# Performance work log

Hardware: AMD Instinct MI355X
Metric: run time of the kernel (lower is better)

Reference implementation:

```python
import math
import jax, jax.numpy as jnp
import numpy as np

N_HEAD = 8
BLOCK_SIZE = 1024
LN_EPS = 1e-5


def _layer_norm(x, g, b):
    mu = jnp.mean(x, axis=-1, keepdims=True)
    var = jnp.var(x, axis=-1, keepdims=True)
    return (x - mu) * jax.lax.rsqrt(var + LN_EPS) * g + b


def _skew(QEr):
    # QEr: (B, nh, L, L) -> pad one zero column on the left, reshape, drop first row
    B, nh, nr, nc = QEr.shape
    padded = jnp.pad(QEr, ((0, 0), (0, 0), (0, 0), (1, 0)))  # (B, nh, nr, nc+1)
    reshaped = padded.reshape(B, nh, nc + 1, nr)
    return reshaped[:, :, 1:, :]  # (B, nh, nr, nc)


def _attn(x, W_qkv, b_qkv, W_o, b_o, Er):
    B, L, D = x.shape
    hs = D // N_HEAD
    qkv = x @ W_qkv + b_qkv  # (B, L, 3D)
    q, k, v = jnp.split(qkv, 3, axis=-1)
    # (B, nh, L, hs)
    q = q.reshape(B, L, N_HEAD, hs).transpose(0, 2, 1, 3)
    k = k.reshape(B, L, N_HEAD, hs).transpose(0, 2, 1, 3)
    v = v.reshape(B, L, N_HEAD, hs).transpose(0, 2, 1, 3)
    start = BLOCK_SIZE - L
    Er_t = Er[start:, :].T  # (hs, L)
    QEr = q @ Er_t  # (B, nh, L, L)
    Srel = _skew(QEr)
    scores = (jnp.einsum('bhqd,bhkd->bhqk', q, k) + Srel) * (1.0 / math.sqrt(hs))
    causal = jnp.tril(jnp.ones((L, L), dtype=bool))
    scores = jnp.where(causal, scores, jnp.float32(-jnp.inf))
    att = jax.nn.softmax(scores, axis=-1)
    y = jnp.einsum('bhqk,bhkd->bhqd', att, v)
    y = y.transpose(0, 2, 1, 3).reshape(B, L, D)
    return y @ W_o + b_o


def reference(x, W_qkv, b_qkv, W_o, b_o, Er, ln1_g, ln1_b, ln2_g, ln2_b,
              W_fc, b_fc, W_proj, b_proj):
    x = x + _attn(_layer_norm(x, ln1_g, ln1_b), W_qkv, b_qkv, W_o, b_o, Er)
    h = _layer_norm(x, ln2_g, ln2_b) @ W_fc + b_fc
    h = jax.nn.gelu(h, approximate=False)
    h = h @ W_proj + b_proj
    return x + h


def setup_inputs() -> dict:
    key = jax.random.key(0)
    ks = jax.random.split(key, 8)
    B, L, D, F = 8, 1024, 1024, 4096
    hs = D // N_HEAD
    s = lambda fan_in: 1.0 / math.sqrt(fan_in)
    return {
        'x': jax.random.normal(ks[0], (B, L, D), dtype=jnp.float32),
        'W_qkv': jax.random.normal(ks[1], (D, 3 * D), dtype=jnp.float32) * s(D),
        'b_qkv': jnp.zeros((3 * D,), dtype=jnp.float32),
        'W_o': jax.random.normal(ks[2], (D, D), dtype=jnp.float32) * s(D),
        'b_o': jnp.zeros((D,), dtype=jnp.float32),
        'Er': jax.random.normal(ks[3], (BLOCK_SIZE, hs), dtype=jnp.float32),
        'ln1_g': jnp.ones((D,), dtype=jnp.float32),
        'ln1_b': jnp.zeros((D,), dtype=jnp.float32),
        'ln2_g': jnp.ones((D,), dtype=jnp.float32),
        'ln2_b': jnp.zeros((D,), dtype=jnp.float32),
        'W_fc': jax.random.normal(ks[4], (D, F), dtype=jnp.float32) * s(D),
        'b_fc': jnp.zeros((F,), dtype=jnp.float32),
        'W_proj': jax.random.normal(ks[5], (F, D), dtype=jnp.float32) * s(F),
        'b_proj': jnp.zeros((D,), dtype=jnp.float32),
    }
```

## Files before the change

kernel.cpp:

```cpp
#include <hip/hip_runtime.h>
#include <hip/hip_bf16.h>
#include <math.h>

#define BB 8
#define LL 1024
#define DD 1024
#define FF 4096
#define NHH 8
#define HSS 128
#define SCALE 0.08838834764831845f
#define TRI(qi, kt) ((qi) * ((qi) + 1) / 2 + (kt))

typedef __bf16 bf16;
typedef __bf16 bf16x8 __attribute__((ext_vector_type(8)));
typedef float f32x4 __attribute__((ext_vector_type(4)));
typedef _Float16 f16;
typedef _Float16 f16x4 __attribute__((ext_vector_type(4)));

__device__ inline void async_copy16(const void* g, void* l) {
  __builtin_amdgcn_global_load_lds(
      (const __attribute__((address_space(1))) unsigned int*)g,
      (__attribute__((address_space(3))) unsigned int*)l, 16, 0, 0);
}

#define FENCE() asm volatile("" ::: "memory")
#define BARRIER() do { FENCE(); __builtin_amdgcn_s_barrier(); FENCE(); } while (0)
#define VMCNT0() asm volatile("s_waitcnt vmcnt(0)" ::: "memory")
#define VMCNT2() asm volatile("s_waitcnt vmcnt(2)" ::: "memory")
#define VMCNT4() asm volatile("s_waitcnt vmcnt(4)" ::: "memory")
#define VMCNT6() asm volatile("s_waitcnt vmcnt(6)" ::: "memory")

__global__ __launch_bounds__(256)
void prep_kernel(const float* __restrict__ Wq, const float* __restrict__ Wo,
                 const float* __restrict__ Wf, const float* __restrict__ Wp,
                 const float* __restrict__ Er, bf16* __restrict__ Wtq,
                 bf16* __restrict__ Wto, bf16* __restrict__ Wtf,
                 bf16* __restrict__ Wtp, bf16* __restrict__ ErP) {
  __shared__ float tile[32][33];
  int id = blockIdx.x, tid = threadIdx.x;
  if (id >= 12288) {
    int g = id - 12288;
    int l15 = tid & 15, quad = (tid >> 4) & 3, st = tid >> 6;
    const float* src = Er + (size_t)(g * 16 + l15) * HSS + st * 32 + quad * 8;
    bf16* dst = ErP + (size_t)g * 2048 + tid * 8;
#pragma unroll
    for (int j = 0; j < 8; j++) dst[j] = (bf16)src[j];
    return;
  }
  const float* W;
  bf16* Wt;
  int K, N, bx, by;
  if (id < 3072)      { W = Wq; Wt = Wtq; K = 1024; N = 3072; bx = id % 96;  by = id / 96; }
  else if (id < 4096) { id -= 3072; W = Wo; Wt = Wto; K = 1024; N = 1024; bx = id % 32;  by = id / 32; }
  else if (id < 8192) { id -= 4096; W = Wf; Wt = Wtf; K = 1024; N = 4096; bx = id % 128; by = id / 128; }
  else                { id -= 8192; W = Wp; Wt = Wtp; K = 4096; N = 1024; bx = id % 32;  by = id / 32; }
  int n0 = bx * 32, k0 = by * 32;
  int tx = tid & 31, ty = tid >> 5;
#pragma unroll
  for (int i = 0; i < 32; i += 8)
    tile[ty + i][tx] = W[(size_t)(k0 + ty + i) * N + n0 + tx];
  __syncthreads();
#pragma unroll
  for (int i = 0; i < 32; i += 8)
    Wt[(size_t)(n0 + ty + i) * K + k0 + tx] = (bf16)tile[tx][ty + i];
}

__global__ __launch_bounds__(256)
void ln_kernel(const float* __restrict__ x, const float* __restrict__ g,
               const float* __restrict__ bta, bf16* __restrict__ out) {
  int row = blockIdx.x;
  int tid = threadIdx.x;
  const float4 v = ((const float4*)(x + (size_t)row * DD))[tid];
  float s = v.x + v.y + v.z + v.w;
  float s2 = v.x * v.x + v.y * v.y + v.z * v.z + v.w * v.w;
#pragma unroll
  for (int o = 32; o > 0; o >>= 1) {
    s += __shfl_down(s, o);
    s2 += __shfl_down(s2, o);
  }
  __shared__ float a1[4], a2[4];
  int wave = tid >> 6;
  if ((tid & 63) == 0) { a1[wave] = s; a2[wave] = s2; }
  __syncthreads();
  s = a1[0] + a1[1] + a1[2] + a1[3];
  s2 = a2[0] + a2[1] + a2[2] + a2[3];
  float mu = s * (1.0f / DD);
  float rstd = rsqrtf(s2 * (1.0f / DD) - mu * mu + 1e-5f);
  float4 gv = ((const float4*)g)[tid];
  float4 bv = ((const float4*)bta)[tid];
  bf16* o4 = out + (size_t)row * DD + tid * 4;
  o4[0] = (bf16)((v.x - mu) * rstd * gv.x + bv.x);
  o4[1] = (bf16)((v.y - mu) * rstd * gv.y + bv.y);
  o4[2] = (bf16)((v.z - mu) * rstd * gv.z + bv.z);
  o4[3] = (bf16)((v.w - mu) * rstd * gv.w + bv.w);
}

template <int EPI>
__global__ __launch_bounds__(512)
void gemm256_kernel(const bf16* __restrict__ A, const bf16* __restrict__ Bt,
                    const float* __restrict__ bias, void* __restrict__ Cout,
                    int M, int N, int K) {
  __shared__ bf16 Als[2][256 * 64];
  __shared__ bf16 Bls[2][256 * 64];
  int tid = threadIdx.x;
  int wave = tid >> 6, lane = tid & 63;
  int l15 = lane & 15, quad = lane >> 4;
  int wmi = wave >> 2, wni = wave & 3;
  int m0 = blockIdx.y * 256, n0 = blockIdx.x * 256;

  int u0 = tid, u1 = tid + 512;
  int r0 = u0 >> 3, c0 = ((u0 & 7) ^ (r0 & 7)) << 3;
  int r1 = u1 >> 3, c1 = ((u1 & 7) ^ (r1 & 7)) << 3;
  const bf16* aB0 = A + (size_t)(m0 + r0) * K + c0;
  const bf16* aB1 = A + (size_t)(m0 + r1) * K + c1;
  const bf16* bB0 = Bt + (size_t)(n0 + r0) * K + c0;
  const bf16* bB1 = Bt + (size_t)(n0 + r1) * K + c1;
  int d0 = u0 * 8, d1 = u1 * 8;

  auto stageA = [&](int b, int h, int t) {
    size_t off = (size_t)h * 128 * K + (size_t)t * 64;
    async_copy16(aB0 + off, &Als[b][h * 8192 + d0]);
    async_copy16(aB1 + off, &Als[b][h * 8192 + d1]);
  };
  auto stageB = [&](int b, int h, int t) {
    size_t off = (size_t)h * 128 * K + (size_t)t * 64;
    async_copy16(bB0 + off, &Bls[b][h * 8192 + d0]);
    async_copy16(bB1 + off, &Bls[b][h * 8192 + d1]);
  };

  f32x4 acc[8][4] = {};
  bf16x8 af[2][4], bfr[2][2][2];

  auto readA = [&](int b, int qm) {
#pragma unroll
    for (int kk = 0; kk < 2; kk++)
#pragma unroll
      for (int mt = 0; mt < 4; mt++) {
        int ra = qm * 128 + wmi * 64 + mt * 16 + l15;
        af[kk][mt] = *(const bf16x8*)&Als[b][ra * 64 + (((kk * 4 + quad) ^ (ra & 7)) << 3)];
      }
  };
  auto readB = [&](int b, int qn) {
#pragma unroll
    for (int kk = 0; kk < 2; kk++)
#pragma unroll
      for (int nt = 0; nt < 2; nt++) {
        int rb = qn * 128 + wni * 32 + nt * 16 + l15;
        bfr[qn][kk][nt] = *(const bf16x8*)&Bls[b][rb * 64 + (((kk * 4 + quad) ^ (rb & 7)) << 3)];
      }
  };
  auto mfma16 = [&](int qm, int qn) {
    __builtin_amdgcn_s_setprio(1);
#pragma unroll
    for (int kk = 0; kk < 2; kk++)
#pragma unroll
      for (int mt = 0; mt < 4; mt++)
#pragma unroll
        for (int nt = 0; nt < 2; nt++)
          acc[qm * 4 + mt][qn * 2 + nt] = __builtin_amdgcn_mfma_f32_16x16x32_bf16(
              af[kk][mt], bfr[qn][kk][nt], acc[qm * 4 + mt][qn * 2 + nt], 0, 0, 0);
    __builtin_amdgcn_s_setprio(0);
  };

  int nk = K >> 6;
  stageA(0, 0, 0); stageB(0, 0, 0); stageB(0, 1, 0); stageA(0, 1, 0);
  stageA(1, 0, 1); stageB(1, 1, 1);
  VMCNT6();
  BARRIER();

  for (int t = 0; t < nk; t += 2) {
#pragma unroll
    for (int uu = 0; uu < 2; uu++) {
      const int tt = t + uu;
      const int cur = uu;
      readA(cur, 0); readB(cur, 0); readB(cur, 1);
      if (tt + 1 < nk) stageB(cur ^ 1, 0, tt + 1);
      BARRIER();
      mfma16(0, 0);
      BARRIER();
      if (tt + 1 < nk) stageA(cur ^ 1, 1, tt + 1);
      VMCNT6();
      BARRIER();
      mfma16(0, 1);
      BARRIER();
      readA(cur, 1);
      if (tt + 2 < nk) stageA(cur, 0, tt + 2);
      BARRIER();
      mfma16(1, 1);
      BARRIER();
      if (tt + 2 < nk) stageB(cur, 1, tt + 2);
      VMCNT6();
      BARRIER();
      mfma16(1, 0);
      BARRIER();
    }
  }

#pragma unroll
  for (int MT = 0; MT < 8; MT++) {
#pragma unroll
    for (int NT = 0; NT < 4; NT++) {
      int col = n0 + (NT >> 1) * 128 + wni * 32 + (NT & 1) * 16 + l15;
      float bv = bias[col];
#pragma unroll
      for (int r = 0; r < 4; r++) {
        int row = m0 + (MT >> 2) * 128 + wmi * 64 + (MT & 3) * 16 + quad * 4 + r;
        float v = acc[MT][NT][r] + bv;
        if (EPI == 1) v = 0.5f * v * (1.0f + erff(v * 0.7071067811865475f));
        ((bf16*)Cout)[(size_t)row * N + col] = (bf16)v;
      }
    }
  }
}

template <int EPI>
__global__ __launch_bounds__(512)
void gemm256n_kernel(const bf16* __restrict__ A, const bf16* __restrict__ Bt,
                     const float* __restrict__ bias, const float* __restrict__ res,
                     void* __restrict__ Cout, int M, int N, int K) {
  __shared__ bf16 Als[2][256 * 64];
  __shared__ bf16 Bls[2][128 * 64];
  int tid = threadIdx.x;
  int wave = tid >> 6, lane = tid & 63;
  int l15 = lane & 15, quad = lane >> 4;
  int wmi = wave >> 2, wni = wave & 3;
  int m0 = blockIdx.y * 256, n0 = blockIdx.x * 128;

  int u0 = tid, u1 = tid + 512;
  int r0 = u0 >> 3, c0 = ((u0 & 7) ^ (r0 & 7)) << 3;
  int r1 = u1 >> 3, c1 = ((u1 & 7) ^ (r1 & 7)) << 3;
  const bf16* aB0 = A + (size_t)(m0 + r0) * K + c0;
  const bf16* aB1 = A + (size_t)(m0 + r1) * K + c1;
  const bf16* bB0 = Bt + (size_t)(n0 + r0) * K + c0;
  const bf16* bB1 = Bt + (size_t)(n0 + r1) * K + c1;
  int d0 = u0 * 8, d1 = u1 * 8;

  auto stageA = [&](int b, int h, int t) {
    size_t off = (size_t)h * 128 * K + (size_t)t * 64;
    async_copy16(aB0 + off, &Als[b][h * 8192 + d0]);
    async_copy16(aB1 + off, &Als[b][h * 8192 + d1]);
  };
  auto stageB = [&](int b, int t) {
    size_t off = (size_t)t * 64;
    async_copy16(bB0 + off, &Bls[b][d0]);
    async_copy16(bB1 + off, &Bls[b][d1]);
  };

  f32x4 acc[8][2] = {};
  bf16x8 af[2][4], bfr[2][2];

  auto readA = [&](int b, int qm) {
#pragma unroll
    for (int kk = 0; kk < 2; kk++)
#pragma unroll
      for (int mt = 0; mt < 4; mt++) {
        int ra = qm * 128 + wmi * 64 + mt * 16 + l15;
        af[kk][mt] = *(const bf16x8*)&Als[b][ra * 64 + (((kk * 4 + quad) ^ (ra & 7)) << 3)];
      }
  };
  auto readB = [&](int b) {
#pragma unroll
    for (int kk = 0; kk < 2; kk++)
#pragma unroll
      for (int nt = 0; nt < 2; nt++) {
        int rb = wni * 32 + nt * 16 + l15;
        bfr[kk][nt] = *(const bf16x8*)&Bls[b][rb * 64 + (((kk * 4 + quad) ^ (rb & 7)) << 3)];
      }
  };
  auto mfma16 = [&](int qm) {
    __builtin_amdgcn_s_setprio(1);
#pragma unroll
    for (int kk = 0; kk < 2; kk++)
#pragma unroll
      for (int mt = 0; mt < 4; mt++)
#pragma unroll
        for (int nt = 0; nt < 2; nt++)
          acc[qm * 4 + mt][nt] = __builtin_amdgcn_mfma_f32_16x16x32_bf16(
              af[kk][mt], bfr[kk][nt], acc[qm * 4 + mt][nt], 0, 0, 0);
    __builtin_amdgcn_s_setprio(0);
  };

  int nk = K >> 6;
  stageB(0, 0); stageB(1, 1); stageA(0, 0, 0); stageA(0, 1, 0);
  VMCNT0();
  BARRIER();

  for (int t = 0; t < nk; t += 2) {
#pragma unroll
    for (int uu = 0; uu < 2; uu++) {
      const int tt = t + uu;
      const int cur = uu;
      readA(cur, 0); readB(cur);
      if (tt + 1 < nk) { stageA(cur ^ 1, 0, tt + 1); VMCNT4(); }
      else { VMCNT0(); }
      BARRIER();
      mfma16(0);
      BARRIER();
      readA(cur, 1);
      if (tt + 1 < nk) stageA(cur ^ 1, 1, tt + 1);
      if (tt + 2 < nk) { stageB(cur, tt + 2); VMCNT4(); }
      else { VMCNT2(); }
      BARRIER();
      mfma16(1);
      BARRIER();
    }
  }

#pragma unroll
  for (int MT = 0; MT < 8; MT++) {
#pragma unroll
    for (int NT = 0; NT < 2; NT++) {
      int col = n0 + wni * 32 + NT * 16 + l15;
      float bv = bias[col];
#pragma unroll
      for (int r = 0; r < 4; r++) {
        int row = m0 + (MT >> 2) * 128 + wmi * 64 + (MT & 3) * 16 + quad * 4 + r;
        float v = acc[MT][NT][r] + bv;
        if (EPI == 1) v = 0.5f * v * (1.0f + erff(v * 0.7071067811865475f));
        if (EPI == 2) {
          v += res[(size_t)row * N + col];
          ((float*)Cout)[(size_t)row * N + col] = v;
        } else {
          ((bf16*)Cout)[(size_t)row * N + col] = (bf16)v;
        }
      }
    }
  }
}

__global__ __launch_bounds__(256)
void pack_v_kernel(const bf16* __restrict__ qkv, bf16* __restrict__ Vpack) {
  __shared__ bf16 Vst[64][132];
  int kt = blockIdx.x, h = blockIdx.y, b = blockIdx.z;
  int tid = threadIdx.x;
  const size_t rs = 3 * DD;
  const bf16* vb = qkv + (size_t)b * LL * rs + (size_t)(kt * 64) * rs + 2 * DD + h * HSS;
  bf16* vp = Vpack + ((size_t)(b * NHH + h) * 16 + kt) * (128 * 64);
#pragma unroll
  for (int i = 0; i < 4; i++) {
    int u = i * 256 + tid;
    int kk = u >> 4, c = u & 15;
    *(bf16x8*)&Vst[kk][c * 8] = *(const bf16x8*)(vb + (size_t)kk * rs + c * 8);
  }
  __syncthreads();
#pragma unroll
  for (int i = 0; i < 4; i++) {
    int u = i * 256 + tid;
    int d = u >> 3, c = u & 7;
    bf16x8 t;
#pragma unroll
    for (int j = 0; j < 8; j++) t[j] = Vst[c * 8 + j][d];
    *(bf16x8*)(vp + d * 64 + ((c ^ (d & 7))) * 8) = t;
  }
}

__global__ __launch_bounds__(256)
void relband_kernel(const bf16* __restrict__ qkv, const bf16* __restrict__ ErP,
                    f16* __restrict__ band) {
  int tid = threadIdx.x, wave = tid >> 6, lane = tid & 63;
  int l15 = lane & 15, quad = lane >> 4;
  int h = blockIdx.y, b = blockIdx.z;
  const size_t rs = 3 * DD;
  const bf16* qbase = qkv + (size_t)b * LL * rs + h * HSS;
  f16* bbase = band + (size_t)(b * NHH + h) * (136 * 4096);

#pragma unroll 1
  for (int ph = 0; ph < 2; ph++) {
    int qb = ph ? 15 - blockIdx.x : blockIdx.x;
    int qw0 = qb * 64 + wave * 16;

    bf16x8 qf[4];
#pragma unroll
    for (int st = 0; st < 4; st++)
      qf[st] = *(const bf16x8*)(qbase + (size_t)(qw0 + l15) * rs + st * 32 + quad * 8);

#pragma unroll 1
    for (int kt = 0; kt <= qb; kt++) {
      int k0 = kt * 64;
      int kmax_off = qw0 + 15 - k0;
      int m_base = 1008 - qw0 + k0;
      int gb = m_base >> 4;
      int ntR = (kmax_off >> 4) + 1;
      if (ntR > 4) ntR = 4;

      f32x4 rr[5] = {};
      __builtin_amdgcn_s_setprio(1);
#pragma unroll
      for (int n = 0; n < 5; n++) {
        if (n <= ntR) {
          int g = gb + n;
          if (g > 63) g = 63;
          const bf16* ep = ErP + (size_t)g * 2048 + lane * 8;
#pragma unroll
          for (int st = 0; st < 4; st++) {
            bf16x8 ef = *(const bf16x8*)(ep + st * 512);
            rr[n] = __builtin_amdgcn_mfma_f32_16x16x32_bf16(qf[st], ef, rr[n], 0, 0, 0);
          }
        }
      }
      __builtin_amdgcn_s_setprio(0);

      f16x4 sf[4];
#pragma unroll
      for (int rg = 0; rg < 4; rg++) {
        int qloc = quad * 4 + rg;
        int tt = 15 - qloc + l15;
        int src = (lane & 48) | (tt & 15);
        float shv[5];
#pragma unroll
        for (int n = 0; n < 5; n++)
          shv[n] = (n <= ntR) ? __shfl(rr[n][rg], src) : 0.f;
#pragma unroll
        for (int nt = 0; nt < 4; nt++)
          sf[nt][rg] = (f16)((tt & 16) ? shv[nt + 1] : shv[nt]);
      }
      f16* tb = bbase + (size_t)TRI(qb, kt) * 4096;
#pragma unroll
      for (int nt = 0; nt < 4; nt++)
        if (nt * 16 <= kmax_off)
          *(f16x4*)(tb + (wave * 4 + nt) * 256 + l15 * 16 + quad * 4) = sf[nt];
    }
  }
}

__global__ __launch_bounds__(256)
void flash_kernel(const bf16* __restrict__ qkv, const bf16* __restrict__ Vpack,
                  const f16* __restrict__ band, bf16* __restrict__ y) {
  __shared__ bf16 Kls[2][64 * 128];
  __shared__ bf16 Vls[2][128 * 64];
  __shared__ bf16 Pls[4][16][72];

  int tid = threadIdx.x, wave = tid >> 6, lane = tid & 63;
  int l15 = lane & 15, quad = lane >> 4;
  int h = blockIdx.y, b = blockIdx.z;

  const size_t rs = 3 * DD;
  const bf16* qbase = qkv + (size_t)b * LL * rs + h * HSS;
  const bf16* kb = qbase + DD;
  const bf16* vp = Vpack + (size_t)(b * NHH + h) * 16 * (128 * 64);
  const f16* bnd = band + (size_t)(b * NHH + h) * (136 * 4096);

  size_t koff[4];
  int ldso[4];
#pragma unroll
  for (int i = 0; i < 4; i++) {
    int off = (wave * 4 + i) * 512 + lane * 8;
    int u = off >> 3;
    int kk = u >> 4, c = u & 15;
    koff[i] = (size_t)kk * rs + (size_t)(((c ^ kk) & 15) * 8);
    ldso[i] = off;
  }

  int buf = 0;
#pragma unroll 1
  for (int ph = 0; ph < 2; ph++) {
    int qb = ph ? 15 - blockIdx.x : blockIdx.x;
    int qw0 = qb * 64 + wave * 16;
    int nkt = qb + 1;

    bf16x8 qf[4];
#pragma unroll
    for (int st = 0; st < 4; st++)
      qf[st] = *(const bf16x8*)(qbase + (size_t)(qw0 + l15) * rs + st * 32 + quad * 8);

#pragma unroll
    for (int i = 0; i < 4; i++) {
      async_copy16(kb + koff[i], &Kls[buf][ldso[i]]);
      async_copy16(vp + ldso[i], &Vls[buf][ldso[i]]);
    }

    f32x4 o[8] = {};
    float mrow[4] = {-INFINITY, -INFINITY, -INFINITY, -INFINITY};
    float lrow[4] = {0.f, 0.f, 0.f, 0.f};

#pragma unroll 1
    for (int kt = 0; kt < nkt; kt++) {
      int k0 = kt * 64;
      int kmax_off = qw0 + 15 - k0;
      __syncthreads();

      const f16* tb = bnd + (size_t)TRI(qb, kt) * 4096;
      f16x4 srl[4] = {};
#pragma unroll
      for (int nt = 0; nt < 4; nt++)
        if (nt * 16 <= kmax_off)
          srl[nt] = *(const f16x4*)(tb + (wave * 4 + nt) * 256 + l15 * 16 + quad * 4);

      if (kt + 1 < nkt) {
        const bf16* ks = kb + (size_t)(kt + 1) * 64 * rs;
        const bf16* vs = vp + (size_t)(kt + 1) * (128 * 64);
#pragma unroll
        for (int i = 0; i < 4; i++) {
          async_copy16(ks + koff[i], &Kls[buf ^ 1][ldso[i]]);
          async_copy16(vs + ldso[i], &Vls[buf ^ 1][ldso[i]]);
        }
      }

      f32x4 sa[4] = {};
      __builtin_amdgcn_s_setprio(1);
#pragma unroll
      for (int nt = 0; nt < 4; nt++) {
        if (nt * 16 <= kmax_off) {
          int kk = nt * 16 + l15;
#pragma unroll
          for (int st = 0; st < 4; st++) {
            bf16x8 kf = *(const bf16x8*)&Kls[buf][kk * 128 + (((st * 4 + quad) ^ l15) & 15) * 8];
            sa[nt] = __builtin_amdgcn_mfma_f32_16x16x32_bf16(qf[st], kf, sa[nt], 0, 0, 0);
          }
        }
      }
      __builtin_amdgcn_s_setprio(0);

      float pmx[4] = {-INFINITY, -INFINITY, -INFINITY, -INFINITY};
#pragma unroll
      for (int nt = 0; nt < 4; nt++) {
        if (nt * 16 <= kmax_off) {
          int kg = k0 + nt * 16 + l15;
#pragma unroll
          for (int rg = 0; rg < 4; rg++) {
            int qg = qw0 + quad * 4 + rg;
            float v = (sa[nt][rg] + (float)srl[nt][rg]) * SCALE;
            v = (kg <= qg) ? v : -INFINITY;
            sa[nt][rg] = v;
            pmx[rg] = fmaxf(pmx[rg], v);
          }
        } else {
#pragma unroll
          for (int rg = 0; rg < 4; rg++) sa[nt][rg] = -INFINITY;
        }
      }

      float vmx[4];
      bool need = false;
#pragma unroll
      for (int rg = 0; rg < 4; rg++) {
        float v = pmx[rg];
        v = fmaxf(v, __shfl_xor(v, 1));
        v = fmaxf(v, __shfl_xor(v, 2));
        v = fmaxf(v, __shfl_xor(v, 4));
        v = fmaxf(v, __shfl_xor(v, 8));
        vmx[rg] = v;
        need = need || (v - mrow[rg] > 8.0f);
      }
      if (__any(need)) {
#pragma unroll
        for (int rg = 0; rg < 4; rg++) {
          float mnew = fmaxf(mrow[rg], vmx[rg]);
          float alpha = __expf(mrow[rg] - mnew);
          mrow[rg] = mnew;
          lrow[rg] *= alpha;
#pragma unroll
          for (int nt = 0; nt < 8; nt++) o[nt][rg] *= alpha;
        }
      }
#pragma unroll
      for (int rg = 0; rg < 4; rg++) pmx[rg] = mrow[rg];

      float ls[4] = {0.f, 0.f, 0.f, 0.f};
#pragma unroll
      for (int nt = 0; nt < 4; nt++)
#pragma unroll
        for (int rg = 0; rg < 4; rg++) {
          float p = __expf(sa[nt][rg] - pmx[rg]);
          ls[rg] += p;
          Pls[wave][quad * 4 + rg][nt * 16 + l15] = (bf16)p;
        }
#pragma unroll
      for (int rg = 0; rg < 4; rg++) {
        float v = ls[rg];
        v += __shfl_xor(v, 1);
        v += __shfl_xor(v, 2);
        v += __shfl_xor(v, 4);
        v += __shfl_xor(v, 8);
        lrow[rg] += v;
      }

      bf16x8 pf[2];
#pragma unroll
      for (int s2 = 0; s2 < 2; s2++)
        pf[s2] = *(const bf16x8*)&Pls[wave][l15][s2 * 32 + quad * 8];
      __builtin_amdgcn_s_setprio(1);
#pragma unroll
      for (int nt = 0; nt < 8; nt++) {
        int d = nt * 16 + l15;
#pragma unroll
        for (int s2 = 0; s2 < 2; s2++) {
          if (s2 * 32 <= kmax_off) {
            bf16x8 vf = *(const bf16x8*)&Vls[buf][d * 64 + (((s2 * 4 + quad) ^ (l15 & 7)) & 7) * 8];
            o[nt] = __builtin_amdgcn_mfma_f32_16x16x32_bf16(pf[s2], vf, o[nt], 0, 0, 0);
          }
        }
      }
      __builtin_amdgcn_s_setprio(0);
      buf ^= 1;
    }

#pragma unroll
    for (int rg = 0; rg < 4; rg++) {
      float inv = 1.0f / lrow[rg];
      int qg = qw0 + quad * 4 + rg;
      bf16* yr = y + ((size_t)b * LL + qg) * DD + h * HSS;
#pragma unroll
      for (int nt = 0; nt < 8; nt++) yr[nt * 16 + l15] = (bf16)(o[nt][rg] * inv);
    }
  }
}

extern "C" void kernel_launch(void* const* d_in, const int* in_sizes, int n_in,
                              void* d_out, int out_size, void* d_ws, size_t ws_size,
                              hipStream_t stream) {
  const float* x = (const float*)d_in[0];
  const float* W_qkv = (const float*)d_in[1];
  const float* b_qkv = (const float*)d_in[2];
  const float* W_o = (const float*)d_in[3];
  const float* b_o = (const float*)d_in[4];
  const float* Er = (const float*)d_in[5];
  const float* ln1_g = (const float*)d_in[6];
  const float* ln1_b = (const float*)d_in[7];
  const float* ln2_g = (const float*)d_in[8];
  const float* ln2_b = (const float*)d_in[9];
  const float* W_fc = (const float*)d_in[10];
  const float* b_fc = (const float*)d_in[11];
  const float* W_proj = (const float*)d_in[12];
  const float* b_proj = (const float*)d_in[13];
  float* out = (float*)d_out;

  char* p = (char*)d_ws;
  auto alloc = [&](size_t bytes) {
    char* r = p;
    p += (bytes + 255) & ~(size_t)255;
    return r;
  };
  bf16* Wt_qkv = (bf16*)alloc((size_t)3072 * 1024 * 2);
  bf16* Wt_o   = (bf16*)alloc((size_t)1024 * 1024 * 2);
  bf16* Wt_fc  = (bf16*)alloc((size_t)4096 * 1024 * 2);
  bf16* Wt_pr  = (bf16*)alloc((size_t)1024 * 4096 * 2);
  bf16* ErP    = (bf16*)alloc((size_t)1024 * 128 * 2);
  bf16* xn     = (bf16*)alloc((size_t)8192 * 1024 * 2);
  bf16* qkvb   = (bf16*)alloc((size_t)8192 * 3072 * 2);
  bf16* yb     = (bf16*)alloc((size_t)8192 * 1024 * 2);
  bf16* Vpack  = (bf16*)alloc((size_t)64 * 16 * 128 * 64 * 2);
  f16*  band   = (f16*)alloc((size_t)64 * 136 * 4096 * 2);
  float* x2    = (float*)band;
  bf16* hb     = qkvb;

  prep_kernel<<<12352, 256, 0, stream>>>(W_qkv, W_o, W_fc, W_proj, Er,
                                         Wt_qkv, Wt_o, Wt_fc, Wt_pr, ErP);

  ln_kernel<<<8192, 256, 0, stream>>>(x, ln1_g, ln1_b, xn);
  gemm256n_kernel<0><<<dim3(24, 32), 512, 0, stream>>>(xn, Wt_qkv, b_qkv, nullptr, qkvb, 8192, 3072, 1024);
  pack_v_kernel<<<dim3(16, 8, 8), 256, 0, stream>>>(qkvb, Vpack);
  relband_kernel<<<dim3(8, 8, 8), 256, 0, stream>>>(qkvb, ErP, band);
  flash_kernel<<<dim3(8, 8, 8), 256, 0, stream>>>(qkvb, Vpack, band, yb);
  gemm256n_kernel<2><<<dim3(8, 32), 512, 0, stream>>>(yb, Wt_o, b_o, x, x2, 8192, 1024, 1024);
  ln_kernel<<<8192, 256, 0, stream>>>(x2, ln2_g, ln2_b, xn);
  gemm256_kernel<1><<<dim3(16, 32), 512, 0, stream>>>(xn, Wt_fc, b_fc, hb, 8192, 4096, 1024);
  gemm256n_kernel<2><<<dim3(8, 32), 512, 0, stream>>>(hb, Wt_pr, b_proj, x2, out, 8192, 1024, 4096);
}
```

Before: 604.6 us.

## Fuse relative-position band computation into flash attention kernel

Removes the separate relband kernel, which computed the skewed Q·Er band and wrote it to global memory as f16. The flash kernel now loads Er tiles itself, runs extra MFMAs per key tile, and does the skew with lane shuffles in registers before masking and softmax. This drops the band write and read-back plus one launch, at the cost of more register pressure (20 extra bf16x8 fragments) and more work inside the attention loop, which may lower occupancy. x2 now gets its own buffer, since it no longer aliases the band.

```diff
diff --git a/kernel.cpp b/kernel.cpp
--- a/kernel.cpp
+++ b/kernel.cpp
@@ -355,36 +355,65 @@
 }
 
 __global__ __launch_bounds__(256)
-void relband_kernel(const bf16* __restrict__ qkv, const bf16* __restrict__ ErP,
-                    f16* __restrict__ band) {
+void flash_kernel(const bf16* __restrict__ qkv, const bf16* __restrict__ Vpack,
+                  const bf16* __restrict__ ErP, bf16* __restrict__ y) {
+  __shared__ bf16 Kls[2][64 * 128];
+  __shared__ bf16 Vls[2][128 * 64];
+  __shared__ bf16 Pls[4][16][72];
+
   int tid = threadIdx.x, wave = tid >> 6, lane = tid & 63;
   int l15 = lane & 15, quad = lane >> 4;
   int h = blockIdx.y, b = blockIdx.z;
+
   const size_t rs = 3 * DD;
   const bf16* qbase = qkv + (size_t)b * LL * rs + h * HSS;
-  f16* bbase = band + (size_t)(b * NHH + h) * (136 * 4096);
-
+  const bf16* kb = qbase + DD;
+  const bf16* vp = Vpack + (size_t)(b * NHH + h) * 16 * (128 * 64);
+
+  size_t koff[4];
+  int ldso[4];
+#pragma unroll
+  for (int i = 0; i < 4; i++) {
+    int off = (wave * 4 + i) * 512 + lane * 8;
+    int u = off >> 3;
+    int kk = u >> 4, c = u & 15;
+    koff[i] = (size_t)kk * rs + (size_t)(((c ^ kk) & 15) * 8);
+    ldso[i] = off;
+  }
+
+  int buf = 0;
 #pragma unroll 1
   for (int ph = 0; ph < 2; ph++) {
     int qb = ph ? 15 - blockIdx.x : blockIdx.x;
     int qw0 = qb * 64 + wave * 16;
+    int nkt = qb + 1;
 
     bf16x8 qf[4];
 #pragma unroll
     for (int st = 0; st < 4; st++)
       qf[st] = *(const bf16x8*)(qbase + (size_t)(qw0 + l15) * rs + st * 32 + quad * 8);
 
+#pragma unroll
+    for (int i = 0; i < 4; i++) {
+      async_copy16(kb + koff[i], &Kls[buf][ldso[i]]);
+      async_copy16(vp + ldso[i], &Vls[buf][ldso[i]]);
+    }
+
+    f32x4 o[8] = {};
+    float mrow[4] = {-INFINITY, -INFINITY, -INFINITY, -INFINITY};
+    float lrow[4] = {0.f, 0.f, 0.f, 0.f};
+
 #pragma unroll 1
-    for (int kt = 0; kt <= qb; kt++) {
+    for (int kt = 0; kt < nkt; kt++) {
       int k0 = kt * 64;
       int kmax_off = qw0 + 15 - k0;
       int m_base = 1008 - qw0 + k0;
       int gb = m_base >> 4;
       int ntR = (kmax_off >> 4) + 1;
       if (ntR > 4) ntR = 4;
-
-      f32x4 rr[5] = {};
-      __builtin_amdgcn_s_setprio(1);
+      __syncthreads();
+
+      bf16x8 ef[5][4];
 #pragma unroll
       for (int n = 0; n < 5; n++) {
         if (n <= ntR) {
@@ -392,99 +421,10 @@
           if (g > 63) g = 63;
           const bf16* ep = ErP + (size_t)g * 2048 + lane * 8;
 #pragma unroll
-          for (int st = 0; st < 4; st++) {
-            bf16x8 ef = *(const bf16x8*)(ep + st * 512);
-            rr[n] = __builtin_amdgcn_mfma_f32_16x16x32_bf16(qf[st], ef, rr[n], 0, 0, 0);
-          }
-        }
-      }
-      __builtin_amdgcn_s_setprio(0);
-
-      f16x4 sf[4];
-#pragma unroll
-      for (int rg = 0; rg < 4; rg++) {
-        int qloc = quad * 4 + rg;
-        int tt = 15 - qloc + l15;
-        int src = (lane & 48) | (tt & 15);
-        float shv[5];
-#pragma unroll
-        for (int n = 0; n < 5; n++)
-          shv[n] = (n <= ntR) ? __shfl(rr[n][rg], src) : 0.f;
-#pragma unroll
-        for (int nt = 0; nt < 4; nt++)
-          sf[nt][rg] = (f16)((tt & 16) ? shv[nt + 1] : shv[nt]);
-      }
-      f16* tb = bbase + (size_t)TRI(qb, kt) * 4096;
-#pragma unroll
-      for (int nt = 0; nt < 4; nt++)
-        if (nt * 16 <= kmax_off)
-          *(f16x4*)(tb + (wave * 4 + nt) * 256 + l15 * 16 + quad * 4) = sf[nt];
-    }
-  }
-}
-
-__global__ __launch_bounds__(256)
-void flash_kernel(const bf16* __restrict__ qkv, const bf16* __restrict__ Vpack,
-                  const f16* __restrict__ band, bf16* __restrict__ y) {
-  __shared__ bf16 Kls[2][64 * 128];
-  __shared__ bf16 Vls[2][128 * 64];
-  __shared__ bf16 Pls[4][16][72];
-
-  int tid = threadIdx.x, wave = tid >> 6, lane = tid & 63;
-  int l15 = lane & 15, quad = lane >> 4;
-  int h = blockIdx.y, b = blockIdx.z;
-
-  const size_t rs = 3 * DD;
-  const bf16* qbase = qkv + (size_t)b * LL * rs + h * HSS;
-  const bf16* kb = qbase + DD;
-  const bf16* vp = Vpack + (size_t)(b * NHH + h) * 16 * (128 * 64);
-  const f16* bnd = band + (size_t)(b * NHH + h) * (136 * 4096);
-
-  size_t koff[4];
-  int ldso[4];
-#pragma unroll
-  for (int i = 0; i < 4; i++) {
-    int off = (wave * 4 + i) * 512 + lane * 8;
-    int u = off >> 3;
-    int kk = u >> 4, c = u & 15;
-    koff[i] = (size_t)kk * rs + (size_t)(((c ^ kk) & 15) * 8);
-    ldso[i] = off;
-  }
-
-  int buf = 0;
-#pragma unroll 1
-  for (int ph = 0; ph < 2; ph++) {
-    int qb = ph ? 15 - blockIdx.x : blockIdx.x;
-    int qw0 = qb * 64 + wave * 16;
-    int nkt = qb + 1;
-
-    bf16x8 qf[4];
-#pragma unroll
-    for (int st = 0; st < 4; st++)
-      qf[st] = *(const bf16x8*)(qbase + (size_t)(qw0 + l15) * rs + st * 32 + quad * 8);
-
-#pragma unroll
-    for (int i = 0; i < 4; i++) {
-      async_copy16(kb + koff[i], &Kls[buf][ldso[i]]);
-      async_copy16(vp + ldso[i], &Vls[buf][ldso[i]]);
-    }
-
-    f32x4 o[8] = {};
-    float mrow[4] = {-INFINITY, -INFINITY, -INFINITY, -INFINITY};
-    float lrow[4] = {0.f, 0.f, 0.f, 0.f};
-
-#pragma unroll 1
-    for (int kt = 0; kt < nkt; kt++) {
-      int k0 = kt * 64;
-      int kmax_off = qw0 + 15 - k0;
-      __syncthreads();
-
-      const f16* tb = bnd + (size_t)TRI(qb, kt) * 4096;
-      f16x4 srl[4] = {};
-#pragma unroll
-      for (int nt = 0; nt < 4; nt++)
-        if (nt * 16 <= kmax_off)
-          srl[nt] = *(const f16x4*)(tb + (wave * 4 + nt) * 256 + l15 * 16 + quad * 4);
+          for (int st = 0; st < 4; st++)
+            ef[n][st] = *(const bf16x8*)(ep + st * 512);
+        }
+      }
 
       if (kt + 1 < nkt) {
         const bf16* ks = kb + (size_t)(kt + 1) * 64 * rs;
@@ -495,6 +435,18 @@
           async_copy16(vs + ldso[i], &Vls[buf ^ 1][ldso[i]]);
         }
       }
+
+      f32x4 rr[5] = {};
+      __builtin_amdgcn_s_setprio(1);
+#pragma unroll
+      for (int n = 0; n < 5; n++) {
+        if (n <= ntR) {
+#pragma unroll
+          for (int st = 0; st < 4; st++)
+            rr[n] = __builtin_amdgcn_mfma_f32_16x16x32_bf16(qf[st], ef[n][st], rr[n], 0, 0, 0);
+        }
+      }
+      __builtin_amdgcn_s_setprio(0);
 
       f32x4 sa[4] = {};
       __builtin_amdgcn_s_setprio(1);
@@ -513,20 +465,27 @@
 
       float pmx[4] = {-INFINITY, -INFINITY, -INFINITY, -INFINITY};
 #pragma unroll
-      for (int nt = 0; nt < 4; nt++) {
-        if (nt * 16 <= kmax_off) {
-          int kg = k0 + nt * 16 + l15;
-#pragma unroll
-          for (int rg = 0; rg < 4; rg++) {
-            int qg = qw0 + quad * 4 + rg;
-            float v = (sa[nt][rg] + (float)srl[nt][rg]) * SCALE;
+      for (int rg = 0; rg < 4; rg++) {
+        int qloc = quad * 4 + rg;
+        int qg = qw0 + qloc;
+        int tt = 15 - qloc + l15;
+        int src = (lane & 48) | (tt & 15);
+        float shv[5];
+#pragma unroll
+        for (int n = 0; n < 5; n++)
+          shv[n] = (n <= ntR) ? __shfl(rr[n][rg], src) : 0.f;
+#pragma unroll
+        for (int nt = 0; nt < 4; nt++) {
+          if (nt * 16 <= kmax_off) {
+            int kg = k0 + nt * 16 + l15;
+            float srel = (tt & 16) ? shv[nt + 1] : shv[nt];
+            float v = (sa[nt][rg] + srel) * SCALE;
             v = (kg <= qg) ? v : -INFINITY;
             sa[nt][rg] = v;
             pmx[rg] = fmaxf(pmx[rg], v);
+          } else {
+            sa[nt][rg] = -INFINITY;
           }
-        } else {
-#pragma unroll
-          for (int rg = 0; rg < 4; rg++) sa[nt][rg] = -INFINITY;
         }
       }
 
@@ -553,15 +512,13 @@
           for (int nt = 0; nt < 8; nt++) o[nt][rg] *= alpha;
         }
       }
-#pragma unroll
-      for (int rg = 0; rg < 4; rg++) pmx[rg] = mrow[rg];
 
       float ls[4] = {0.f, 0.f, 0.f, 0.f};
 #pragma unroll
       for (int nt = 0; nt < 4; nt++)
 #pragma unroll
         for (int rg = 0; rg < 4; rg++) {
-          float p = __expf(sa[nt][rg] - pmx[rg]);
+          float p = __expf(sa[nt][rg] - mrow[rg]);
           ls[rg] += p;
           Pls[wave][quad * 4 + rg][nt * 16 + l15] = (bf16)p;
         }
@@ -640,8 +597,7 @@
   bf16* qkvb   = (bf16*)alloc((size_t)8192 * 3072 * 2);
   bf16* yb     = (bf16*)alloc((size_t)8192 * 1024 * 2);
   bf16* Vpack  = (bf16*)alloc((size_t)64 * 16 * 128 * 64 * 2);
-  f16*  band   = (f16*)alloc((size_t)64 * 136 * 4096 * 2);
-  float* x2    = (float*)band;
+  float* x2    = (float*)alloc((size_t)8192 * 1024 * 4);
   bf16* hb     = qkvb;
 
   prep_kernel<<<12352, 256, 0, stream>>>(W_qkv, W_o, W_fc, W_proj, Er,
@@ -650,8 +606,7 @@
   ln_kernel<<<8192, 256, 0, stream>>>(x, ln1_g, ln1_b, xn);
   gemm256n_kernel<0><<<dim3(24, 32), 512, 0, stream>>>(xn, Wt_qkv, b_qkv, nullptr, qkvb, 8192, 3072, 1024);
   pack_v_kernel<<<dim3(16, 8, 8), 256, 0, stream>>>(qkvb, Vpack);
-  relband_kernel<<<dim3(8, 8, 8), 256, 0, stream>>>(qkvb, ErP, band);
-  flash_kernel<<<dim3(8, 8, 8), 256, 0, stream>>>(qkvb, Vpack, band, yb);
+  flash_kernel<<<dim3(8, 8, 8), 256, 0, stream>>>(qkvb, Vpack, ErP, yb);
   gemm256n_kernel<2><<<dim3(8, 32), 512, 0, stream>>>(yb, Wt_o, b_o, x, x2, 8192, 1024, 1024);
   ln_kernel<<<8192, 256, 0, stream>>>(x2, ln2_g, ln2_b, xn);
   gemm256_kernel<1><<<dim3(16, 32), 512, 0, stream>>>(xn, Wt_fc, b_fc, hb, 8192, 4096, 1024);
```

Measured after the change: 795.1 us. 31.5% more time.
